# Kernel tuning notes

Hardware: AMD Instinct MI355X
Metric: run time of the kernel (lower is better)

The kernel has to match this reference:

```python
import jax, jax.numpy as jnp
import numpy as np

B, S, D, H = 2048, 48, 256, 8   # graphs, nodes per graph, hidden dim, attention heads
DH = D // H
STEPS = 4
NEG_SLOPE = 0.2  # leaky_relu slope used by GAT attention


def setup_inputs() -> dict:
    key = jax.random.key(0)
    ks = jax.random.split(key, 10)
    gl = lambda i, shape: jax.random.normal(ks[i], shape, jnp.float32) * (1.0 / np.sqrt(shape[0]))
    return dict(
        node_feature=jax.random.normal(ks[0], (B * S, D), jnp.float32),
        graph_indicator=jnp.repeat(jnp.arange(B, dtype=jnp.int32), S),
        gat_kernel=gl(1, (D, D)),
        gat_self_kernel=gl(2, (D, D)),
        att_src=jax.random.normal(ks[3], (H, DH), jnp.float32) * 0.1,
        att_dst=jax.random.normal(ks[4], (H, DH), jnp.float32) * 0.1,
        gru_wx=gl(5, (D, 3 * D)),
        gru_wh=gl(6, (D, 3 * D)),
        gru_bx=jnp.zeros((3 * D,), jnp.float32),
        gru_bh=jnp.zeros((3 * D,), jnp.float32),
        proj_w=gl(7, (D, D)),
        proj_b=jnp.zeros((D,), jnp.float32),
    )


def _gru_cell(x, h, wx, wh, bx, bh):
    # keras GRUCell (reset_after=True): separate input/recurrent biases
    xz, xr, xh = jnp.split(x @ wx + bx, 3, axis=-1)
    hz, hr, hh = jnp.split(h @ wh + bh, 3, axis=-1)
    z = jax.nn.sigmoid(xz + hz)
    r = jax.nn.sigmoid(xr + hr)
    n = jnp.tanh(xh + r * hh)
    return z * h + (1.0 - z) * n


def reference(node_feature, graph_indicator, gat_kernel, gat_self_kernel,
              att_src, att_dst, gru_wx, gru_wh, gru_bx, gru_bh, proj_w, proj_b):
    # --- _add_virtual_super_nodes: prepend per-graph virtual node = sum of node features
    x_real = node_feature.reshape(B, S, D)
    virtual = jnp.sum(x_real, axis=1, keepdims=True)           # [B,1,D]
    x = jnp.concatenate([virtual, x_real], axis=1)             # [B,S+1,D]; index 0 = virtual node
    state = x[:, 0]                                            # gathered virtual node state [B,D]

    for _ in range(STEPS):
        # --- GATConv message step over star edges (real node s -> virtual node 0)
        h = (x @ gat_kernel).reshape(B, S + 1, H, DH)          # projected node features
        e_src = jnp.einsum('bshd,hd->bsh', h[:, 1:], att_src)  # per-edge src score
        e_dst = jnp.einsum('bhd,hd->bh', h[:, 0], att_dst)     # dst (virtual) score
        e = jax.nn.leaky_relu(e_src + e_dst[:, None, :], NEG_SLOPE)
        alpha = jax.nn.softmax(e, axis=1)                      # segment softmax over edge_dst
        msg = jnp.einsum('bsh,bshd->bhd', alpha, h[:, 1:]).reshape(B, D)
        # only virtual nodes receive messages; real nodes aggregate zero
        agg = jnp.concatenate([msg[:, None], jnp.zeros((B, S, D), x.dtype)], axis=1)
        out = jax.nn.relu(agg + x @ gat_self_kernel)           # self-projection + activation

        # --- gather virtual node feature, GRUCell update, scatter back
        state = _gru_cell(out[:, 0], state, gru_wx, gru_wh, gru_bx, gru_bh)
        x = out.at[:, 0].set(state)

    # --- final node projection of virtual node state -> molecule embedding [B,D]
    return state @ proj_w + proj_b
```

## Files before the change

### kernel.cpp

```cpp
#include <hip/hip_runtime.h>
#include <hip/hip_bf16.h>
#include <stdint.h>


#define NEG_SLOPE 0.2f

typedef unsigned short u16;
typedef short s16x8 __attribute__((ext_vector_type(8)));
typedef float f32x4 __attribute__((ext_vector_type(4)));
typedef float f32x2 __attribute__((ext_vector_type(2)));
typedef u16 u16x2 __attribute__((ext_vector_type(2)));
typedef u16 u16x4 __attribute__((ext_vector_type(4)));
typedef u16 u16x8 __attribute__((ext_vector_type(8)));

__device__ __forceinline__ u16 f2bf(float f) {
  union { float f; uint32_t u; } v; v.f = f;
  uint32_t r = (v.u + 0x7FFFu + ((v.u >> 16) & 1u)) >> 16;
  return (u16)r;
}
__device__ __forceinline__ float bf2f(u16 h) {
  union { uint32_t u; float f; } v; v.u = ((uint32_t)h) << 16;
  return v.f;
}

__device__ __forceinline__ void gload_lds16(const void* g, void* l) {
  __builtin_amdgcn_global_load_lds(
      (const __attribute__((address_space(1))) void*)g,
      (__attribute__((address_space(3))) void*)l, 16, 0, 0);
}

__device__ __forceinline__ float redsum_lk(float v) {
  v += __shfl_xor(v, 16); v += __shfl_xor(v, 32);
  return v;
}
__device__ __forceinline__ float redmax_lk(float v) {
  v = fmaxf(v, __shfl_xor(v, 16)); v = fmaxf(v, __shfl_xor(v, 32));
  return v;
}
__device__ __forceinline__ float redsum_wave(float v) {
  v += __shfl_xor(v, 1); v += __shfl_xor(v, 2); v += __shfl_xor(v, 4);
  v += __shfl_xor(v, 8); v += __shfl_xor(v, 16); v += __shfl_xor(v, 32);
  return v;
}

template<int NS>
__global__ __launch_bounds__(128, 2)
void fused_step(const u16* __restrict__ X, const u16* __restrict__ BP,
                const u16* __restrict__ EP, const float* __restrict__ SV,
                const float* __restrict__ ED, u16* __restrict__ GS,
                u16* __restrict__ Xn) {
  __shared__ u16 ldsB[2][8192];
  __shared__ float alphaL[2][8][48];
  const int tid = threadIdx.x;
  const int w = tid >> 6, l = tid & 63, lr = l & 15, lk = l >> 4;
  const int b = blockIdx.x * 2 + w;
  const u16* Xg = X + (size_t)b * 48 * 256;

#define STAGE(S, BUF)                                                          \
  {                                                                            \
    _Pragma("unroll") for (int i_ = 0; i_ < 8; ++i_)                           \
        gload_lds16(BP + ((size_t)(S)*1024 + i_ * 128 + tid) * 8,              \
                    &ldsB[BUF][(i_ * 128 + w * 64) * 8]);                      \
  }

  s16x8 af[8][3];
#pragma unroll
  for (int kc = 0; kc < 8; ++kc)
#pragma unroll
    for (int mi = 0; mi < 3; ++mi)
      af[kc][mi] = *(const s16x8*)(Xg + (size_t)(mi * 16 + lr) * 256 + kc * 32 + lk * 8);

  s16x8 be[8];
#pragma unroll
  for (int kc = 0; kc < 8; ++kc)
    be[kc] = *(const s16x8*)(EP + ((size_t)kc * 64 + l) * 8);

  const float edv = ED[(size_t)b * 8 + (l & 7)];
  f32x2 svA[8];
#pragma unroll
  for (int h = 0; h < 8; ++h)
    svA[h] = *(const f32x2*)(SV + (size_t)b * 256 + h * 32 + 2 * lr);

  asm volatile("s_waitcnt vmcnt(0)" ::: "memory");
  STAGE(0, 0)

  {
    f32x4 ae[3];
#pragma unroll
    for (int mi = 0; mi < 3; ++mi) ae[mi] = (f32x4){0.f, 0.f, 0.f, 0.f};
#pragma unroll
    for (int kc = 0; kc < 8; ++kc)
#pragma unroll
      for (int mi = 0; mi < 3; ++mi)
        ae[mi] = __builtin_amdgcn_mfma_f32_16x16x32_bf16(af[kc][mi], be[kc], ae[mi], 0, 0, 0);

    if (lr < 8) {
      float ev[3][4];
      float m = -1e30f;
#pragma unroll
      for (int mi = 0; mi < 3; ++mi)
#pragma unroll
        for (int j = 0; j < 4; ++j) {
          float v = ae[mi][j] + edv;
          v = (v > 0.f) ? v : NEG_SLOPE * v;
          ev[mi][j] = v;
          m = fmaxf(m, v);
        }
      m = redmax_lk(m);
      float sm = 0.f;
#pragma unroll
      for (int mi = 0; mi < 3; ++mi)
#pragma unroll
        for (int j = 0; j < 4; ++j) {
          float ex = expf(ev[mi][j] - m);
          ev[mi][j] = ex; sm += ex;
        }
      sm = redsum_lk(sm);
      const float inv = 1.f / sm;
#pragma unroll
      for (int mi = 0; mi < 3; ++mi)
#pragma unroll
        for (int j = 0; j < 4; ++j)
          alphaL[w][lr][mi * 16 + lk * 4 + j] = ev[mi][j] * inv;
    }
  }

#pragma unroll
  for (int s = 0; s < NS; ++s) {
    if (s == 0)      { asm volatile("s_waitcnt vmcnt(0)" ::: "memory"); }
    else if (s <= 8) { asm volatile("s_waitcnt vmcnt(1)" ::: "memory"); }
    else             { asm volatile("s_waitcnt vmcnt(12)" ::: "memory"); }
    __builtin_amdgcn_s_barrier();
    if (s + 1 < NS) STAGE(s + 1, (s + 1) & 1)

    f32x4 acc[3][2];
#pragma unroll
    for (int mi = 0; mi < 3; ++mi)
#pragma unroll
      for (int ni = 0; ni < 2; ++ni) acc[mi][ni] = (f32x4){0.f, 0.f, 0.f, 0.f};

    const u16* bufB = ldsB[s & 1];
#pragma unroll
    for (int kc = 0; kc < 8; ++kc) {
      s16x8 bfr[2];
#pragma unroll
      for (int ni = 0; ni < 2; ++ni)
        bfr[ni] = *(const s16x8*)&bufB[((kc * 2 + ni) * 64 + l) * 8];
#pragma unroll
      for (int mi = 0; mi < 3; ++mi)
#pragma unroll
        for (int ni = 0; ni < 2; ++ni)
          acc[mi][ni] = __builtin_amdgcn_mfma_f32_16x16x32_bf16(
              af[kc][mi], bfr[ni], acc[mi][ni], 0, 0, 0);
    }

    if (s < 8) {
      float mm0 = 0.f, mm1 = 0.f;
#pragma unroll
      for (int mi = 0; mi < 3; ++mi)
#pragma unroll
        for (int j = 0; j < 4; ++j) {
          const float a = alphaL[w][s][mi * 16 + lk * 4 + j];
          mm0 += a * acc[mi][0][j];
          mm1 += a * acc[mi][1][j];
        }
      mm0 = redsum_lk(mm0);
      mm1 = redsum_lk(mm1);
      if (lk == 0) {
        u16x2 o = {f2bf(fmaxf(mm0 + svA[s][0], 0.f)),
                   f2bf(fmaxf(mm1 + svA[s][1], 0.f))};
        *(u16x2*)(GS + (size_t)b * 512 + s * 32 + 2 * lr) = o;
      }
    } else {
#pragma unroll
      for (int mi = 0; mi < 3; ++mi)
#pragma unroll
        for (int j = 0; j < 4; ++j) {
          u16x2 o = {f2bf(fmaxf(acc[mi][0][j], 0.f)),
                     f2bf(fmaxf(acc[mi][1][j], 0.f))};
          *(u16x2*)(Xn + (size_t)(b * 48 + mi * 16 + lk * 4 + j) * 256 +
                    (s - 8) * 32 + 2 * lr) = o;
        }
    }
  }
#undef STAGE
}

template<int EPI>
__global__ __launch_bounds__(256)
void gemm_bt(const u16* __restrict__ A, int lda,
             const u16* __restrict__ Bt,
             float* __restrict__ Cf, int ldc, const float* __restrict__ bias) {
  __shared__ u16 ldsA[2][2 * 128 * 32];
  __shared__ u16 ldsB[2][2 * 128 * 32];
  const int tid = threadIdx.x;
  const int w = tid >> 6, l = tid & 63;
  const int wr = w >> 1, wc = w & 1;
  const int lr = l & 15, lk = l >> 4;
  const int sxor = (lr >> 1) & 3;
  const int m0 = blockIdx.x * 128, n0 = blockIdx.y * 128;

#define STAGE_AB(KT, BUF)                                                      \
  {                                                                            \
    const u16* Ag = A + (size_t)m0 * lda + (KT)*64;                            \
    const u16* Bg = Bt + (size_t)n0 * 256 + (KT)*64;                           \
    _Pragma("unroll") for (int i = 0; i < 4; ++i) {                            \
      int q = i * 256 + tid;                                                   \
      int h2 = q >> 9, r = (q >> 2) & 127, c4 = q & 3;                         \
      int c4s = c4 ^ ((r >> 1) & 3);                                           \
      gload_lds16(Ag + (size_t)r * lda + h2 * 32 + c4s * 8,                    \
                  &ldsA[BUF][(i * 256 + w * 64) * 8]);                         \
      gload_lds16(Bg + (size_t)r * 256 + h2 * 32 + c4s * 8,                    \
                  &ldsB[BUF][(i * 256 + w * 64) * 8]);                         \
    }                                                                          \
  }

  f32x4 acc[4][4];
#pragma unroll
  for (int i = 0; i < 4; ++i)
#pragma unroll
    for (int j = 0; j < 4; ++j) acc[i][j] = (f32x4){0.f, 0.f, 0.f, 0.f};

  STAGE_AB(0, 0)
#pragma unroll
  for (int kt = 0; kt < 4; ++kt) {
    __syncthreads();
    if (kt < 3) STAGE_AB(kt + 1, (kt + 1) & 1)
    const u16* bA = ldsA[kt & 1];
    const u16* bB = ldsB[kt & 1];
#pragma unroll
    for (int hh = 0; hh < 2; ++hh) {
      s16x8 af[4], bfr[4];
#pragma unroll
      for (int mi = 0; mi < 4; ++mi)
        af[mi] = *(const s16x8*)&bA[(hh * 128 + wr * 64 + mi * 16 + lr) * 32 +
                                    (lk ^ sxor) * 8];
#pragma unroll
      for (int ni = 0; ni < 4; ++ni)
        bfr[ni] = *(const s16x8*)&bB[(hh * 128 + wc * 64 + ni * 16 + lr) * 32 +
                                     (lk ^ sxor) * 8];
#pragma unroll
      for (int mi = 0; mi < 4; ++mi)
#pragma unroll
        for (int ni = 0; ni < 4; ++ni)
          acc[mi][ni] = __builtin_amdgcn_mfma_f32_16x16x32_bf16(af[mi], bfr[ni],
                                                                acc[mi][ni], 0, 0, 0);
    }
  }
#undef STAGE_AB

#pragma unroll
  for (int mi = 0; mi < 4; ++mi) {
#pragma unroll
    for (int ni = 0; ni < 4; ++ni) {
      f32x4 v = acc[mi][ni];
      int r = m0 + wr * 64 + mi * 16 + lk * 4;
      int c = n0 + wc * 64 + ni * 16 + lr;
#pragma unroll
      for (int j = 0; j < 4; ++j) {
        float fv = v[j];
        if (EPI == 0) Cf[(size_t)(r + j) * ldc + c] = fv;
        else          Cf[(size_t)(r + j) * ldc + c] = fv + bias[c];
      }
    }
  }
}

__global__ __launch_bounds__(256)
void gemm_gates(const u16* __restrict__ GS, const u16* __restrict__ WXT,
                const u16* __restrict__ WHT, float* __restrict__ G1,
                float* __restrict__ G2) {
  __shared__ u16 ldsA[2][2 * 128 * 32];
  __shared__ u16 ldsB[2][2 * 128 * 32];
  const bool second = blockIdx.y >= 6;
  const u16* A = GS + (second ? 256 : 0);
  const u16* Bt = second ? WHT : WXT;
  float* Cf = second ? G2 : G1;
  const int n0 = (second ? blockIdx.y - 6 : blockIdx.y) * 128;
  const int m0 = blockIdx.x * 128;
  const int tid = threadIdx.x;
  const int w = tid >> 6, l = tid & 63;
  const int wr = w >> 1, wc = w & 1;
  const int lr = l & 15, lk = l >> 4;
  const int sxor = (lr >> 1) & 3;

#define STAGE_AB(KT, BUF)                                                      \
  {                                                                            \
    const u16* Ag = A + (size_t)m0 * 512 + (KT)*64;                            \
    const u16* Bg = Bt + (size_t)n0 * 256 + (KT)*64;                           \
    _Pragma("unroll") for (int i = 0; i < 4; ++i) {                            \
      int q = i * 256 + tid;                                                   \
      int h2 = q >> 9, r = (q >> 2) & 127, c4 = q & 3;                         \
      int c4s = c4 ^ ((r >> 1) & 3);                                           \
      gload_lds16(Ag + (size_t)r * 512 + h2 * 32 + c4s * 8,                    \
                  &ldsA[BUF][(i * 256 + w * 64) * 8]);                         \
      gload_lds16(Bg + (size_t)r * 256 + h2 * 32 + c4s * 8,                    \
                  &ldsB[BUF][(i * 256 + w * 64) * 8]);                         \
    }                                                                          \
  }

  f32x4 acc[4][4];
#pragma unroll
  for (int i = 0; i < 4; ++i)
#pragma unroll
    for (int j = 0; j < 4; ++j) acc[i][j] = (f32x4){0.f, 0.f, 0.f, 0.f};

  STAGE_AB(0, 0)
#pragma unroll
  for (int kt = 0; kt < 4; ++kt) {
    __syncthreads();
    if (kt < 3) STAGE_AB(kt + 1, (kt + 1) & 1)
    const u16* bA = ldsA[kt & 1];
    const u16* bB = ldsB[kt & 1];
#pragma unroll
    for (int hh = 0; hh < 2; ++hh) {
      s16x8 af[4], bfr[4];
#pragma unroll
      for (int mi = 0; mi < 4; ++mi)
        af[mi] = *(const s16x8*)&bA[(hh * 128 + wr * 64 + mi * 16 + lr) * 32 +
                                    (lk ^ sxor) * 8];
#pragma unroll
      for (int ni = 0; ni < 4; ++ni)
        bfr[ni] = *(const s16x8*)&bB[(hh * 128 + wc * 64 + ni * 16 + lr) * 32 +
                                     (lk ^ sxor) * 8];
#pragma unroll
      for (int mi = 0; mi < 4; ++mi)
#pragma unroll
        for (int ni = 0; ni < 4; ++ni)
          acc[mi][ni] = __builtin_amdgcn_mfma_f32_16x16x32_bf16(af[mi], bfr[ni],
                                                                acc[mi][ni], 0, 0, 0);
    }
  }
#undef STAGE_AB

#pragma unroll
  for (int mi = 0; mi < 4; ++mi) {
#pragma unroll
    for (int ni = 0; ni < 4; ++ni) {
      f32x4 v = acc[mi][ni];
      int r = m0 + wr * 64 + mi * 16 + lk * 4;
      int c = n0 + wc * 64 + ni * 16 + lr;
#pragma unroll
      for (int j = 0; j < 4; ++j)
        Cf[(size_t)(r + j) * 768 + c] = v[j];
    }
  }
}

__global__ void pack_all(const float* __restrict__ Ws, const float* __restrict__ wx,
                         const float* __restrict__ wh, const float* __restrict__ pw,
                         u16* __restrict__ WST, u16* __restrict__ WXT,
                         u16* __restrict__ WHT, u16* __restrict__ PRJ) {
  int idx = blockIdx.x * 256 + threadIdx.x;
  const float* src; u16* dst; int N; int li;
  if (idx < 65536)        { src = Ws; dst = WST; N = 256; li = idx; }
  else if (idx < 262144)  { src = wx; dst = WXT; N = 768; li = idx - 65536; }
  else if (idx < 458752)  { src = wh; dst = WHT; N = 768; li = idx - 262144; }
  else                    { src = pw; dst = PRJ; N = 256; li = idx - 458752; }
  int n = li >> 8, k = li & 255;
  dst[li] = f2bf(src[(size_t)k * N + n]);
}

__global__ void pack_bp(const float* __restrict__ Wg, const float* __restrict__ Ws,
                        u16* __restrict__ BP) {
  int c = blockIdx.x * 256 + threadIdx.x;
  int l = c & 63, ni = (c >> 6) & 1, kc = (c >> 7) & 7, s = c >> 10;
  int n = s * 32 + ((l & 15) << 1) + ni;
  int k0 = kc * 32 + (l >> 4) * 8;
  const float* W = (n < 256) ? Wg : Ws;
  int nn = n & 255;
  u16x8 o;
#pragma unroll
  for (int e = 0; e < 8; ++e) o[e] = f2bf(W[(size_t)(k0 + e) * 256 + nn]);
  *(u16x8*)(BP + (size_t)c * 8) = o;
}

__global__ void wgad_kernel(const float* __restrict__ Wg, const float* __restrict__ adst,
                            const float* __restrict__ asrc,
                            float* __restrict__ WGAD, float* __restrict__ WGAS) {
  const int h = blockIdx.x, d = threadIdx.x;
  float sd = 0.f, ss = 0.f;
#pragma unroll
  for (int j = 0; j < 32; ++j) {
    float wv = Wg[(size_t)d * 256 + h * 32 + j];
    sd += wv * adst[h * 32 + j];
    ss += wv * asrc[h * 32 + j];
  }
  WGAD[(size_t)d * 8 + h] = sd;
  WGAS[(size_t)d * 8 + h] = ss;
}

__global__ void pack_ep(const float* __restrict__ WGAS, u16* __restrict__ EP) {
  int c = blockIdx.x * 256 + threadIdx.x;
  if (c >= 512) return;
  int l = c & 63, kc = c >> 6;
  int hh = l & 15, k0 = kc * 32 + (l >> 4) * 8;
  u16x8 o;
#pragma unroll
  for (int e = 0; e < 8; ++e)
    o[e] = (hh < 8) ? f2bf(WGAS[(size_t)(k0 + e) * 8 + hh]) : (u16)0;
  *(u16x8*)(EP + (size_t)c * 8) = o;
}

__global__ __launch_bounds__(256)
void prep_x_kernel(const float* __restrict__ nf, u16* __restrict__ X0,
                   float* __restrict__ state, u16* __restrict__ GS,
                   const float* __restrict__ WGAD, float* __restrict__ ED) {
  __shared__ f32x4 part[4][64];
  __shared__ float stt[256];
  __shared__ float red[4][8];
  const int b = blockIdx.x, t = threadIdx.x;
  const int c4 = t & 63, sg = t >> 6, l = t & 63;
  const f32x4* src = (const f32x4*)(nf + (size_t)b * 48 * 256);
  f32x4 acc = (f32x4){0.f, 0.f, 0.f, 0.f};
  for (int s = sg * 12; s < sg * 12 + 12; ++s) {
    f32x4 v = src[(size_t)s * 64 + c4];
    acc += v;
    u16x4 o = {f2bf(v[0]), f2bf(v[1]), f2bf(v[2]), f2bf(v[3])};
    *(u16x4*)(X0 + ((size_t)b * 48 + s) * 256 + c4 * 4) = o;
  }
  part[sg][c4] = acc;
  __syncthreads();
  if (t < 64) {
    f32x4 r = part[0][t] + part[1][t] + part[2][t] + part[3][t];
#pragma unroll
    for (int j = 0; j < 4; ++j) {
      int d = t * 4 + j;
      stt[d] = r[j];
      state[(size_t)b * 256 + d] = r[j];
      GS[(size_t)b * 512 + 256 + d] = f2bf(r[j]);
    }
  }
  __syncthreads();
  const float st = stt[t];
  float pr[8];
#pragma unroll
  for (int h = 0; h < 8; ++h) pr[h] = redsum_wave(st * WGAD[(size_t)t * 8 + h]);
  if (l == 0) {
#pragma unroll
    for (int h = 0; h < 8; ++h) red[sg][h] = pr[h];
  }
  __syncthreads();
  if (t < 8) ED[(size_t)b * 8 + t] = red[0][t] + red[1][t] + red[2][t] + red[3][t];
}

__global__ void gru_kernel(const float* __restrict__ G1, const float* __restrict__ G2,
                           const float* __restrict__ bx, const float* __restrict__ bh,
                           float* __restrict__ state, u16* __restrict__ GS,
                           const float* __restrict__ WGAD, float* __restrict__ ED) {
  __shared__ float red[4][8];
  const int b = blockIdx.x, d = threadIdx.x;
  const int wv = d >> 6, l = d & 63;
  const float* g1 = G1 + (size_t)b * 768;
  const float* g2 = G2 + (size_t)b * 768;
  float xz = g1[d] + bx[d], xr = g1[256 + d] + bx[256 + d], xh = g1[512 + d] + bx[512 + d];
  float hz = g2[d] + bh[d], hr = g2[256 + d] + bh[256 + d], hh2 = g2[512 + d] + bh[512 + d];
  float z = 1.f / (1.f + expf(-(xz + hz)));
  float r = 1.f / (1.f + expf(-(xr + hr)));
  float n = tanhf(xh + r * hh2);
  float h0 = state[b * 256 + d];
  float sn = z * h0 + (1.f - z) * n;
  state[b * 256 + d] = sn;
  GS[(size_t)b * 512 + 256 + d] = f2bf(sn);
  float pr[8];
#pragma unroll
  for (int h = 0; h < 8; ++h) pr[h] = redsum_wave(sn * WGAD[(size_t)d * 8 + h]);
  if (l == 0) {
#pragma unroll
    for (int h = 0; h < 8; ++h) red[wv][h] = pr[h];
  }
  __syncthreads();
  if (d < 8) ED[(size_t)b * 8 + d] = red[0][d] + red[1][d] + red[2][d] + red[3][d];
}

extern "C" void kernel_launch(void* const* d_in, const int* in_sizes, int n_in,
                              void* d_out, int out_size, void* d_ws, size_t ws_size,
                              hipStream_t stream) {
  const float* nf  = (const float*)d_in[0];
  const float* Wg  = (const float*)d_in[2];
  const float* Ws  = (const float*)d_in[3];
  const float* asr = (const float*)d_in[4];
  const float* ads = (const float*)d_in[5];
  const float* wx  = (const float*)d_in[6];
  const float* wh  = (const float*)d_in[7];
  const float* bx  = (const float*)d_in[8];
  const float* bh  = (const float*)d_in[9];
  const float* pw  = (const float*)d_in[10];
  const float* pb  = (const float*)d_in[11];
  float* out = (float*)d_out;

  char* p = (char*)d_ws;
  size_t off = 0;
  auto alloc = [&](size_t bytes) { char* r = p + off; off += (bytes + 255) & ~255ULL; return r; };
  u16* WST   = (u16*)alloc(256 * 256 * 2);
  u16* WXT   = (u16*)alloc(768 * 256 * 2);
  u16* WHT   = (u16*)alloc(768 * 256 * 2);
  u16* PRJ   = (u16*)alloc(256 * 256 * 2);
  u16* BP    = (u16*)alloc(512 * 256 * 2);
  u16* EP    = (u16*)alloc(512 * 8 * 2);
  float* WGAD = (float*)alloc(256 * 8 * 4);
  float* WGAS = (float*)alloc(256 * 8 * 4);
  u16* X0    = (u16*)alloc((size_t)98304 * 256 * 2);
  u16* X1    = (u16*)alloc((size_t)98304 * 256 * 2);
  float* SV   = (float*)alloc((size_t)2048 * 256 * 4);
  float* ED   = (float*)alloc((size_t)2048 * 8 * 4);
  float* G1   = (float*)alloc((size_t)2048 * 768 * 4);
  float* G2   = (float*)alloc((size_t)2048 * 768 * 4);
  u16* GS     = (u16*)alloc((size_t)2048 * 512 * 2);
  float* ST   = (float*)alloc((size_t)2048 * 256 * 4);

  pack_all<<<2048, 256, 0, stream>>>(Ws, wx, wh, pw, WST, WXT, WHT, PRJ);
  pack_bp<<<64, 256, 0, stream>>>(Wg, Ws, BP);
  wgad_kernel<<<8, 256, 0, stream>>>(Wg, ads, asr, WGAD, WGAS);
  pack_ep<<<2, 256, 0, stream>>>(WGAS, EP);
  prep_x_kernel<<<2048, 256, 0, stream>>>(nf, X0, ST, GS, WGAD, ED);

  u16* xc = X0; u16* xn = X1;
  for (int t = 0; t < 4; ++t) {
    gemm_bt<0><<<dim3(16, 2), 256, 0, stream>>>(GS + 256, 512, WST, SV, 256, nullptr);
    if (t < 3) fused_step<16><<<1024, 128, 0, stream>>>(xc, BP, EP, SV, ED, GS, xn);
    else       fused_step<8><<<1024, 128, 0, stream>>>(xc, BP, EP, SV, ED, GS, nullptr);
    gemm_gates<<<dim3(16, 12), 256, 0, stream>>>(GS, WXT, WHT, G1, G2);
    gru_kernel<<<2048, 256, 0, stream>>>(G1, G2, bx, bh, ST, GS, WGAD, ED);
    u16* tmp = xc; xc = xn; xn = tmp;
  }
  gemm_bt<2><<<dim3(16, 2), 256, 0, stream>>>(GS + 256, 512, PRJ, out, 256, pb);
}
```

Before: 254.0 us.

## Give each wave private LDS weight buffers and drop block barriers in fused_step

Splits the shared B-weight staging buffer into per-wave halves so each wave loads its own copy of each weight slice and needs no s_barrier. Stages are halved to 16 output columns each, so twice as many stages run, with even/odd accumulators combined at the epilogue. The weight packing layout changes to match. This removes cross-wave synchronisation, but each wave now loads its own copy of the weights, doubling global-to-LDS traffic. Odd stages also wait for vmcnt(0), which limits prefetch overlap.

```diff
diff --git a/kernel.cpp b/kernel.cpp
--- a/kernel.cpp
+++ b/kernel.cpp
@@ -49,7 +49,7 @@
                 const u16* __restrict__ EP, const float* __restrict__ SV,
                 const float* __restrict__ ED, u16* __restrict__ GS,
                 u16* __restrict__ Xn) {
-  __shared__ u16 ldsB[2][8192];
+  __shared__ u16 ldsB[2][2][4096];
   __shared__ float alphaL[2][8][48];
   const int tid = threadIdx.x;
   const int w = tid >> 6, l = tid & 63, lr = l & 15, lk = l >> 4;
@@ -59,8 +59,8 @@
 #define STAGE(S, BUF)                                                          \
   {                                                                            \
     _Pragma("unroll") for (int i_ = 0; i_ < 8; ++i_)                           \
-        gload_lds16(BP + ((size_t)(S)*1024 + i_ * 128 + tid) * 8,              \
-                    &ldsB[BUF][(i_ * 128 + w * 64) * 8]);                      \
+        gload_lds16(BP + ((size_t)(S)*512 + i_ * 64 + l) * 8,                  \
+                    &ldsB[w][BUF][i_ * 512]);                                  \
   }
 
   s16x8 af[8][3];
@@ -125,64 +125,65 @@
     }
   }
 
-#pragma unroll
-  for (int s = 0; s < NS; ++s) {
-    if (s == 0)      { asm volatile("s_waitcnt vmcnt(0)" ::: "memory"); }
-    else if (s <= 8) { asm volatile("s_waitcnt vmcnt(1)" ::: "memory"); }
-    else             { asm volatile("s_waitcnt vmcnt(12)" ::: "memory"); }
-    __builtin_amdgcn_s_barrier();
-    if (s + 1 < NS) STAGE(s + 1, (s + 1) & 1)
-
-    f32x4 acc[3][2];
-#pragma unroll
-    for (int mi = 0; mi < 3; ++mi)
-#pragma unroll
-      for (int ni = 0; ni < 2; ++ni) acc[mi][ni] = (f32x4){0.f, 0.f, 0.f, 0.f};
-
-    const u16* bufB = ldsB[s & 1];
-#pragma unroll
-    for (int kc = 0; kc < 8; ++kc) {
-      s16x8 bfr[2];
-#pragma unroll
-      for (int ni = 0; ni < 2; ++ni)
-        bfr[ni] = *(const s16x8*)&bufB[((kc * 2 + ni) * 64 + l) * 8];
-#pragma unroll
-      for (int mi = 0; mi < 3; ++mi)
-#pragma unroll
-        for (int ni = 0; ni < 2; ++ni)
-          acc[mi][ni] = __builtin_amdgcn_mfma_f32_16x16x32_bf16(
-              af[kc][mi], bfr[ni], acc[mi][ni], 0, 0, 0);
-    }
-
-    if (s < 8) {
-      float mm0 = 0.f, mm1 = 0.f;
-#pragma unroll
-      for (int mi = 0; mi < 3; ++mi)
-#pragma unroll
-        for (int j = 0; j < 4; ++j) {
-          const float a = alphaL[w][s][mi * 16 + lk * 4 + j];
-          mm0 += a * acc[mi][0][j];
-          mm1 += a * acc[mi][1][j];
+  f32x4 accE[3], accO[3];
+
+#define CONSUME(ACC, BUF)                                                      \
+  {                                                                            \
+    _Pragma("unroll") for (int mi = 0; mi < 3; ++mi)                           \
+        ACC[mi] = (f32x4){0.f, 0.f, 0.f, 0.f};                                 \
+    const u16* bufB = &ldsB[w][BUF][0];                                        \
+    _Pragma("unroll") for (int kc = 0; kc < 8; ++kc) {                         \
+      s16x8 bfr = *(const s16x8*)&bufB[kc * 512 + l * 8];                      \
+      _Pragma("unroll") for (int mi = 0; mi < 3; ++mi)                         \
+        ACC[mi] = __builtin_amdgcn_mfma_f32_16x16x32_bf16(af[kc][mi], bfr,     \
+                                                          ACC[mi], 0, 0, 0);   \
+    }                                                                          \
+  }
+
+#pragma unroll
+  for (int f = 0; f < NS; ++f) {
+    if (f == 0 || (f & 1)) { asm volatile("s_waitcnt vmcnt(0)" ::: "memory"); }
+    else if (f <= 16)      { asm volatile("s_waitcnt vmcnt(1)" ::: "memory"); }
+    else                   { asm volatile("s_waitcnt vmcnt(12)" ::: "memory"); }
+    if (f + 1 < NS) STAGE(f + 1, (f + 1) & 1)
+
+    if ((f & 1) == 0) {
+      CONSUME(accE, f & 1)
+    } else {
+      CONSUME(accO, f & 1)
+      if (f < 16) {
+        const int h = f >> 1;
+        float mmE = 0.f, mmO = 0.f;
+#pragma unroll
+        for (int mi = 0; mi < 3; ++mi)
+#pragma unroll
+          for (int j = 0; j < 4; ++j) {
+            const float a = alphaL[w][h][mi * 16 + lk * 4 + j];
+            mmE += a * accE[mi][j];
+            mmO += a * accO[mi][j];
+          }
+        mmE = redsum_lk(mmE);
+        mmO = redsum_lk(mmO);
+        if (lk == 0) {
+          u16x2 o = {f2bf(fmaxf(mmE + svA[h][0], 0.f)),
+                     f2bf(fmaxf(mmO + svA[h][1], 0.f))};
+          *(u16x2*)(GS + (size_t)b * 512 + h * 32 + 2 * lr) = o;
         }
-      mm0 = redsum_lk(mm0);
-      mm1 = redsum_lk(mm1);
-      if (lk == 0) {
-        u16x2 o = {f2bf(fmaxf(mm0 + svA[s][0], 0.f)),
-                   f2bf(fmaxf(mm1 + svA[s][1], 0.f))};
-        *(u16x2*)(GS + (size_t)b * 512 + s * 32 + 2 * lr) = o;
+      } else {
+        const int u = (f >> 1) - 8;
+#pragma unroll
+        for (int mi = 0; mi < 3; ++mi)
+#pragma unroll
+          for (int j = 0; j < 4; ++j) {
+            u16x2 o = {f2bf(fmaxf(accE[mi][j], 0.f)),
+                       f2bf(fmaxf(accO[mi][j], 0.f))};
+            *(u16x2*)(Xn + (size_t)(b * 48 + mi * 16 + lk * 4 + j) * 256 +
+                      u * 32 + 2 * lr) = o;
+          }
       }
-    } else {
-#pragma unroll
-      for (int mi = 0; mi < 3; ++mi)
-#pragma unroll
-        for (int j = 0; j < 4; ++j) {
-          u16x2 o = {f2bf(fmaxf(acc[mi][0][j], 0.f)),
-                     f2bf(fmaxf(acc[mi][1][j], 0.f))};
-          *(u16x2*)(Xn + (size_t)(b * 48 + mi * 16 + lk * 4 + j) * 256 +
-                    (s - 8) * 32 + 2 * lr) = o;
-        }
-    }
-  }
+    }
+  }
+#undef CONSUME
 #undef STAGE
 }
 
@@ -364,8 +365,9 @@
 __global__ void pack_bp(const float* __restrict__ Wg, const float* __restrict__ Ws,
                         u16* __restrict__ BP) {
   int c = blockIdx.x * 256 + threadIdx.x;
-  int l = c & 63, ni = (c >> 6) & 1, kc = (c >> 7) & 7, s = c >> 10;
-  int n = s * 32 + ((l & 15) << 1) + ni;
+  int l = c & 63, kc = (c >> 6) & 7, s = c >> 9;
+  int u = s >> 1, p = s & 1;
+  int n = u * 32 + ((l & 15) << 1) + p;
   int k0 = kc * 32 + (l >> 4) * 8;
   const float* W = (n < 256) ? Wg : Ws;
   int nn = n & 255;
@@ -518,8 +520,8 @@
   u16* xc = X0; u16* xn = X1;
   for (int t = 0; t < 4; ++t) {
     gemm_bt<0><<<dim3(16, 2), 256, 0, stream>>>(GS + 256, 512, WST, SV, 256, nullptr);
-    if (t < 3) fused_step<16><<<1024, 128, 0, stream>>>(xc, BP, EP, SV, ED, GS, xn);
-    else       fused_step<8><<<1024, 128, 0, stream>>>(xc, BP, EP, SV, ED, GS, nullptr);
+    if (t < 3) fused_step<32><<<1024, 128, 0, stream>>>(xc, BP, EP, SV, ED, GS, xn);
+    else       fused_step<16><<<1024, 128, 0, stream>>>(xc, BP, EP, SV, ED, GS, nullptr);
     gemm_gates<<<dim3(16, 12), 256, 0, stream>>>(GS, WXT, WHT, G1, G2);
     gru_kernel<<<2048, 256, 0, stream>>>(G1, G2, bx, bh, ST, GS, WGAD, ED);
     u16* tmp = xc; xc = xn; xn = tmp;
```

Result: slower. 264.2 us (+4.0%).

## Fold virtual-node self projection and dst score into fused step MFMA

Applied to the files above, without the earlier changes.

The virtual-node state row is added as a fourth MFMA row tile in the fused step kernel. That tile computes the self-projection (previously a separate gemm_bt launch writing SV) and the destination attention score (previously a wave reduction in the prep and GRU kernels writing ED). The stage order is reordered so the self-kernel columns are processed first and their results are available before the attention aggregation passes. This removes one launch per step and the SV/ED round trips, in exchange for extra MFMA work on a mostly padded 16-row tile and a more complex wait-count schedule.

```diff
diff --git a/kernel.cpp b/kernel.cpp
--- a/kernel.cpp
+++ b/kernel.cpp
@@ -37,17 +37,11 @@
   v = fmaxf(v, __shfl_xor(v, 16)); v = fmaxf(v, __shfl_xor(v, 32));
   return v;
 }
-__device__ __forceinline__ float redsum_wave(float v) {
-  v += __shfl_xor(v, 1); v += __shfl_xor(v, 2); v += __shfl_xor(v, 4);
-  v += __shfl_xor(v, 8); v += __shfl_xor(v, 16); v += __shfl_xor(v, 32);
-  return v;
-}
-
-template<int NS>
+
+template<bool LAST>
 __global__ __launch_bounds__(128, 2)
 void fused_step(const u16* __restrict__ X, const u16* __restrict__ BP,
-                const u16* __restrict__ EP, const float* __restrict__ SV,
-                const float* __restrict__ ED, u16* __restrict__ GS,
+                const u16* __restrict__ EP, u16* __restrict__ GS,
                 u16* __restrict__ Xn) {
   __shared__ u16 ldsB[2][8192];
   __shared__ float alphaL[2][8][48];
@@ -55,6 +49,7 @@
   const int w = tid >> 6, l = tid & 63, lr = l & 15, lk = l >> 4;
   const int b = blockIdx.x * 2 + w;
   const u16* Xg = X + (size_t)b * 48 * 256;
+  const u16* Sg = GS + (size_t)b * 512 + 256;
 
 #define STAGE(S, BUF)                                                          \
   {                                                                            \
@@ -63,36 +58,34 @@
                     &ldsB[BUF][(i_ * 128 + w * 64) * 8]);                      \
   }
 
-  s16x8 af[8][3];
-#pragma unroll
-  for (int kc = 0; kc < 8; ++kc)
+  s16x8 af[8][4];
+#pragma unroll
+  for (int kc = 0; kc < 8; ++kc) {
 #pragma unroll
     for (int mi = 0; mi < 3; ++mi)
       af[kc][mi] = *(const s16x8*)(Xg + (size_t)(mi * 16 + lr) * 256 + kc * 32 + lk * 8);
+    af[kc][3] = *(const s16x8*)(Sg + kc * 32 + lk * 8);
+  }
 
   s16x8 be[8];
 #pragma unroll
   for (int kc = 0; kc < 8; ++kc)
     be[kc] = *(const s16x8*)(EP + ((size_t)kc * 64 + l) * 8);
 
-  const float edv = ED[(size_t)b * 8 + (l & 7)];
-  f32x2 svA[8];
-#pragma unroll
-  for (int h = 0; h < 8; ++h)
-    svA[h] = *(const f32x2*)(SV + (size_t)b * 256 + h * 32 + 2 * lr);
-
   asm volatile("s_waitcnt vmcnt(0)" ::: "memory");
-  STAGE(0, 0)
+  STAGE(8, 0)
 
   {
-    f32x4 ae[3];
-#pragma unroll
-    for (int mi = 0; mi < 3; ++mi) ae[mi] = (f32x4){0.f, 0.f, 0.f, 0.f};
+    f32x4 ae[4];
+#pragma unroll
+    for (int mi = 0; mi < 4; ++mi) ae[mi] = (f32x4){0.f, 0.f, 0.f, 0.f};
 #pragma unroll
     for (int kc = 0; kc < 8; ++kc)
 #pragma unroll
-      for (int mi = 0; mi < 3; ++mi)
+      for (int mi = 0; mi < 4; ++mi)
         ae[mi] = __builtin_amdgcn_mfma_f32_16x16x32_bf16(af[kc][mi], be[kc], ae[mi], 0, 0, 0);
+
+    const float edv = __shfl(ae[3][0], 8 + lr);
 
     if (lr < 8) {
       float ev[3][4];
@@ -125,62 +118,96 @@
     }
   }
 
-#pragma unroll
-  for (int s = 0; s < NS; ++s) {
-    if (s == 0)      { asm volatile("s_waitcnt vmcnt(0)" ::: "memory"); }
-    else if (s <= 8) { asm volatile("s_waitcnt vmcnt(1)" ::: "memory"); }
-    else             { asm volatile("s_waitcnt vmcnt(12)" ::: "memory"); }
+  f32x2 svA[8];
+
+#pragma unroll
+  for (int f = 0; f < 16; ++f) {
+    if (f == 0)       { asm volatile("s_waitcnt vmcnt(0)" ::: "memory"); }
+    else if (f <= 8)  {
+      if (LAST)       { asm volatile("s_waitcnt vmcnt(0)" ::: "memory"); }
+      else            { asm volatile("s_waitcnt vmcnt(12)" ::: "memory"); }
+    } else            { asm volatile("s_waitcnt vmcnt(1)" ::: "memory"); }
     __builtin_amdgcn_s_barrier();
-    if (s + 1 < NS) STAGE(s + 1, (s + 1) & 1)
-
-    f32x4 acc[3][2];
-#pragma unroll
-    for (int mi = 0; mi < 3; ++mi)
-#pragma unroll
-      for (int ni = 0; ni < 2; ++ni) acc[mi][ni] = (f32x4){0.f, 0.f, 0.f, 0.f};
-
-    const u16* bufB = ldsB[s & 1];
-#pragma unroll
-    for (int kc = 0; kc < 8; ++kc) {
-      s16x8 bfr[2];
-#pragma unroll
-      for (int ni = 0; ni < 2; ++ni)
-        bfr[ni] = *(const s16x8*)&bufB[((kc * 2 + ni) * 64 + l) * 8];
-#pragma unroll
-      for (int mi = 0; mi < 3; ++mi)
+    if (f + 1 < 16) {
+      const int ns = (f + 1 < 8) ? (9 + f) : (f + 1 - 8);
+      STAGE(ns, (f + 1) & 1)
+    }
+
+    const u16* bufB = ldsB[f & 1];
+
+    if (f < 8) {
+      f32x4 acc[4][2];
+#pragma unroll
+      for (int mi = 0; mi < 4; ++mi)
+#pragma unroll
+        for (int ni = 0; ni < 2; ++ni) acc[mi][ni] = (f32x4){0.f, 0.f, 0.f, 0.f};
+#pragma unroll
+      for (int kc = 0; kc < 8; ++kc) {
+        s16x8 bfr[2];
 #pragma unroll
         for (int ni = 0; ni < 2; ++ni)
-          acc[mi][ni] = __builtin_amdgcn_mfma_f32_16x16x32_bf16(
-              af[kc][mi], bfr[ni], acc[mi][ni], 0, 0, 0);
-    }
-
-    if (s < 8) {
-      float mm0 = 0.f, mm1 = 0.f;
-#pragma unroll
-      for (int mi = 0; mi < 3; ++mi)
-#pragma unroll
-        for (int j = 0; j < 4; ++j) {
-          const float a = alphaL[w][s][mi * 16 + lk * 4 + j];
-          mm0 += a * acc[mi][0][j];
-          mm1 += a * acc[mi][1][j];
+          bfr[ni] = *(const s16x8*)&bufB[((kc * 2 + ni) * 64 + l) * 8];
+        if (!LAST) {
+#pragma unroll
+          for (int mi = 0; mi < 3; ++mi)
+#pragma unroll
+            for (int ni = 0; ni < 2; ++ni)
+              acc[mi][ni] = __builtin_amdgcn_mfma_f32_16x16x32_bf16(
+                  af[kc][mi], bfr[ni], acc[mi][ni], 0, 0, 0);
         }
-      mm0 = redsum_lk(mm0);
-      mm1 = redsum_lk(mm1);
-      if (lk == 0) {
-        u16x2 o = {f2bf(fmaxf(mm0 + svA[s][0], 0.f)),
-                   f2bf(fmaxf(mm1 + svA[s][1], 0.f))};
-        *(u16x2*)(GS + (size_t)b * 512 + s * 32 + 2 * lr) = o;
+#pragma unroll
+        for (int ni = 0; ni < 2; ++ni)
+          acc[3][ni] = __builtin_amdgcn_mfma_f32_16x16x32_bf16(
+              af[kc][3], bfr[ni], acc[3][ni], 0, 0, 0);
+      }
+      svA[f] = (f32x2){acc[3][0][0], acc[3][1][0]};
+      if (!LAST) {
+#pragma unroll
+        for (int mi = 0; mi < 3; ++mi)
+#pragma unroll
+          for (int j = 0; j < 4; ++j) {
+            u16x2 o = {f2bf(fmaxf(acc[mi][0][j], 0.f)),
+                       f2bf(fmaxf(acc[mi][1][j], 0.f))};
+            *(u16x2*)(Xn + (size_t)(b * 48 + mi * 16 + lk * 4 + j) * 256 +
+                      f * 32 + 2 * lr) = o;
+          }
       }
     } else {
+      const int h = f - 8;
+      f32x4 acc[3][2];
 #pragma unroll
       for (int mi = 0; mi < 3; ++mi)
 #pragma unroll
+        for (int ni = 0; ni < 2; ++ni) acc[mi][ni] = (f32x4){0.f, 0.f, 0.f, 0.f};
+#pragma unroll
+      for (int kc = 0; kc < 8; ++kc) {
+        s16x8 bfr[2];
+#pragma unroll
+        for (int ni = 0; ni < 2; ++ni)
+          bfr[ni] = *(const s16x8*)&bufB[((kc * 2 + ni) * 64 + l) * 8];
+#pragma unroll
+        for (int mi = 0; mi < 3; ++mi)
+#pragma unroll
+          for (int ni = 0; ni < 2; ++ni)
+            acc[mi][ni] = __builtin_amdgcn_mfma_f32_16x16x32_bf16(
+                af[kc][mi], bfr[ni], acc[mi][ni], 0, 0, 0);
+      }
+      float mmE = 0.f, mmO = 0.f;
+#pragma unroll
+      for (int mi = 0; mi < 3; ++mi)
+#pragma unroll
         for (int j = 0; j < 4; ++j) {
-          u16x2 o = {f2bf(fmaxf(acc[mi][0][j], 0.f)),
-                     f2bf(fmaxf(acc[mi][1][j], 0.f))};
-          *(u16x2*)(Xn + (size_t)(b * 48 + mi * 16 + lk * 4 + j) * 256 +
-                    (s - 8) * 32 + 2 * lr) = o;
+          const float a = alphaL[w][h][mi * 16 + lk * 4 + j];
+          mmE += a * acc[mi][0][j];
+          mmO += a * acc[mi][1][j];
         }
+      mmE = redsum_lk(mmE);
+      mmO = redsum_lk(mmO);
+      if (lk == 0) {
+        u16x2 o = {f2bf(fmaxf(mmE + svA[h][0], 0.f)),
+                   f2bf(fmaxf(mmO + svA[h][1], 0.f))};
+        *(u16x2*)(GS + (size_t)b * 512 + h * 32 + 2 * lr) = o;
+      }
     }
   }
 #undef STAGE
@@ -347,16 +374,15 @@
   }
 }
 
-__global__ void pack_all(const float* __restrict__ Ws, const float* __restrict__ wx,
-                         const float* __restrict__ wh, const float* __restrict__ pw,
-                         u16* __restrict__ WST, u16* __restrict__ WXT,
-                         u16* __restrict__ WHT, u16* __restrict__ PRJ) {
+__global__ void pack_all(const float* __restrict__ wx, const float* __restrict__ wh,
+                         const float* __restrict__ pw,
+                         u16* __restrict__ WXT, u16* __restrict__ WHT,
+                         u16* __restrict__ PRJ) {
   int idx = blockIdx.x * 256 + threadIdx.x;
   const float* src; u16* dst; int N; int li;
-  if (idx < 65536)        { src = Ws; dst = WST; N = 256; li = idx; }
-  else if (idx < 262144)  { src = wx; dst = WXT; N = 768; li = idx - 65536; }
-  else if (idx < 458752)  { src = wh; dst = WHT; N = 768; li = idx - 262144; }
-  else                    { src = pw; dst = PRJ; N = 256; li = idx - 458752; }
+  if (idx < 196608)       { src = wx; dst = WXT; N = 768; li = idx; }
+  else if (idx < 393216)  { src = wh; dst = WHT; N = 768; li = idx - 196608; }
+  else                    { src = pw; dst = PRJ; N = 256; li = idx - 393216; }
   int n = li >> 8, k = li & 255;
   dst[li] = f2bf(src[(size_t)k * N + n]);
 }
@@ -390,7 +416,8 @@
   WGAS[(size_t)d * 8 + h] = ss;
 }
 
-__global__ void pack_ep(const float* __restrict__ WGAS, u16* __restrict__ EP) {
+__global__ void pack_ep(const float* __restrict__ WGAS, const float* __restrict__ WGAD,
+                        u16* __restrict__ EP) {
   int c = blockIdx.x * 256 + threadIdx.x;
   if (c >= 512) return;
   int l = c & 63, kc = c >> 6;
@@ -398,19 +425,17 @@
   u16x8 o;
 #pragma unroll
   for (int e = 0; e < 8; ++e)
-    o[e] = (hh < 8) ? f2bf(WGAS[(size_t)(k0 + e) * 8 + hh]) : (u16)0;
+    o[e] = (hh < 8) ? f2bf(WGAS[(size_t)(k0 + e) * 8 + hh])
+                    : f2bf(WGAD[(size_t)(k0 + e) * 8 + (hh - 8)]);
   *(u16x8*)(EP + (size_t)c * 8) = o;
 }
 
 __global__ __launch_bounds__(256)
 void prep_x_kernel(const float* __restrict__ nf, u16* __restrict__ X0,
-                   float* __restrict__ state, u16* __restrict__ GS,
-                   const float* __restrict__ WGAD, float* __restrict__ ED) {
+                   float* __restrict__ state, u16* __restrict__ GS) {
   __shared__ f32x4 part[4][64];
-  __shared__ float stt[256];
-  __shared__ float red[4][8];
   const int b = blockIdx.x, t = threadIdx.x;
-  const int c4 = t & 63, sg = t >> 6, l = t & 63;
+  const int c4 = t & 63, sg = t >> 6;
   const f32x4* src = (const f32x4*)(nf + (size_t)b * 48 * 256);
   f32x4 acc = (f32x4){0.f, 0.f, 0.f, 0.f};
   for (int s = sg * 12; s < sg * 12 + 12; ++s) {
@@ -426,31 +451,16 @@
 #pragma unroll
     for (int j = 0; j < 4; ++j) {
       int d = t * 4 + j;
-      stt[d] = r[j];
       state[(size_t)b * 256 + d] = r[j];
       GS[(size_t)b * 512 + 256 + d] = f2bf(r[j]);
     }
   }
-  __syncthreads();
-  const float st = stt[t];
-  float pr[8];
-#pragma unroll
-  for (int h = 0; h < 8; ++h) pr[h] = redsum_wave(st * WGAD[(size_t)t * 8 + h]);
-  if (l == 0) {
-#pragma unroll
-    for (int h = 0; h < 8; ++h) red[sg][h] = pr[h];
-  }
-  __syncthreads();
-  if (t < 8) ED[(size_t)b * 8 + t] = red[0][t] + red[1][t] + red[2][t] + red[3][t];
 }
 
 __global__ void gru_kernel(const float* __restrict__ G1, const float* __restrict__ G2,
                            const float* __restrict__ bx, const float* __restrict__ bh,
-                           float* __restrict__ state, u16* __restrict__ GS,
-                           const float* __restrict__ WGAD, float* __restrict__ ED) {
-  __shared__ float red[4][8];
+                           float* __restrict__ state, u16* __restrict__ GS) {
   const int b = blockIdx.x, d = threadIdx.x;
-  const int wv = d >> 6, l = d & 63;
   const float* g1 = G1 + (size_t)b * 768;
   const float* g2 = G2 + (size_t)b * 768;
   float xz = g1[d] + bx[d], xr = g1[256 + d] + bx[256 + d], xh = g1[512 + d] + bx[512 + d];
@@ -462,15 +472,6 @@
   float sn = z * h0 + (1.f - z) * n;
   state[b * 256 + d] = sn;
   GS[(size_t)b * 512 + 256 + d] = f2bf(sn);
-  float pr[8];
-#pragma unroll
-  for (int h = 0; h < 8; ++h) pr[h] = redsum_wave(sn * WGAD[(size_t)d * 8 + h]);
-  if (l == 0) {
-#pragma unroll
-    for (int h = 0; h < 8; ++h) red[wv][h] = pr[h];
-  }
-  __syncthreads();
-  if (d < 8) ED[(size_t)b * 8 + d] = red[0][d] + red[1][d] + red[2][d] + red[3][d];
 }
 
 extern "C" void kernel_launch(void* const* d_in, const int* in_sizes, int n_in,
@@ -492,7 +493,6 @@
   char* p = (char*)d_ws;
   size_t off = 0;
   auto alloc = [&](size_t bytes) { char* r = p + off; off += (bytes + 255) & ~255ULL; return r; };
-  u16* WST   = (u16*)alloc(256 * 256 * 2);
   u16* WXT   = (u16*)alloc(768 * 256 * 2);
   u16* WHT   = (u16*)alloc(768 * 256 * 2);
   u16* PRJ   = (u16*)alloc(256 * 256 * 2);
@@ -502,26 +502,23 @@
   float* WGAS = (float*)alloc(256 * 8 * 4);
   u16* X0    = (u16*)alloc((size_t)98304 * 256 * 2);
   u16* X1    = (u16*)alloc((size_t)98304 * 256 * 2);
-  float* SV   = (float*)alloc((size_t)2048 * 256 * 4);
-  float* ED   = (float*)alloc((size_t)2048 * 8 * 4);
   float* G1   = (float*)alloc((size_t)2048 * 768 * 4);
   float* G2   = (float*)alloc((size_t)2048 * 768 * 4);
   u16* GS     = (u16*)alloc((size_t)2048 * 512 * 2);
   float* ST   = (float*)alloc((size_t)2048 * 256 * 4);
 
-  pack_all<<<2048, 256, 0, stream>>>(Ws, wx, wh, pw, WST, WXT, WHT, PRJ);
+  pack_all<<<1792, 256, 0, stream>>>(wx, wh, pw, WXT, WHT, PRJ);
   pack_bp<<<64, 256, 0, stream>>>(Wg, Ws, BP);
   wgad_kernel<<<8, 256, 0, stream>>>(Wg, ads, asr, WGAD, WGAS);
-  pack_ep<<<2, 256, 0, stream>>>(WGAS, EP);
-  prep_x_kernel<<<2048, 256, 0, stream>>>(nf, X0, ST, GS, WGAD, ED);
+  pack_ep<<<2, 256, 0, stream>>>(WGAS, WGAD, EP);
+  prep_x_kernel<<<2048, 256, 0, stream>>>(nf, X0, ST, GS);
 
   u16* xc = X0; u16* xn = X1;
   for (int t = 0; t < 4; ++t) {
-    gemm_bt<0><<<dim3(16, 2), 256, 0, stream>>>(GS + 256, 512, WST, SV, 256, nullptr);
-    if (t < 3) fused_step<16><<<1024, 128, 0, stream>>>(xc, BP, EP, SV, ED, GS, xn);
-    else       fused_step<8><<<1024, 128, 0, stream>>>(xc, BP, EP, SV, ED, GS, nullptr);
+    if (t < 3) fused_step<false><<<1024, 128, 0, stream>>>(xc, BP, EP, GS, xn);
+    else       fused_step<true ><<<1024, 128, 0, stream>>>(xc, BP, EP, GS, nullptr);
     gemm_gates<<<dim3(16, 12), 256, 0, stream>>>(GS, WXT, WHT, G1, G2);
-    gru_kernel<<<2048, 256, 0, stream>>>(G1, G2, bx, bh, ST, GS, WGAD, ED);
+    gru_kernel<<<2048, 256, 0, stream>>>(G1, G2, bx, bh, ST, GS);
     u16* tmp = xc; xc = xn; xn = tmp;
   }
   gemm_bt<2><<<dim3(16, 2), 256, 0, stream>>>(GS + 256, 512, PRJ, out, 256, pb);
```

After: 225.7 us. -11.1%, faster.
